# Performance work log

Measured on AMD Instinct MI355X. Metric: run time of the kernel, lower is better.

## Reference

```python
import jax, jax.numpy as jnp
import numpy as np

B, Q, K, H, V = 32, 64, 512, 64, 64
NEG = -1e6


def setup_inputs() -> dict:
    key = jax.random.key(0)
    ks = jax.random.split(key, 7)
    queries = jax.random.normal(ks[0], (B, Q, H), dtype=jnp.float32)
    keys = jax.random.normal(ks[1], (B, K, H), dtype=jnp.float32)
    values = jax.random.normal(ks[2], (B, K, V), dtype=jnp.float32)
    valid_lens = jax.random.randint(ks[3], (B,), 1, K + 1, dtype=jnp.int32)
    # Linear weights stored as (in_features, out_features); x @ W == torch Linear
    Wq = jax.random.normal(ks[4], (H, H), dtype=jnp.float32) / np.sqrt(H)
    Wk = jax.random.normal(ks[5], (H, H), dtype=jnp.float32) / np.sqrt(H)
    wv = jax.random.normal(ks[6], (H,), dtype=jnp.float32) / np.sqrt(H)
    return {"queries": queries, "keys": keys, "values": values,
            "valid_lens": valid_lens, "Wq": Wq, "Wk": Wk, "wv": wv}


def reference(queries, keys, values, valid_lens, Wq, Wk, wv):
    q = jnp.einsum('bqd,dh->bqh', queries, Wq)          # (B,Q,H)
    k = jnp.einsum('bkd,dh->bkh', keys, Wk)             # (B,K,H)
    # additive (Bahdanau) features: (B,Q,K,H) broadcast intermediate
    feats = jnp.tanh(q[:, :, None, :] + k[:, None, :, :])
    scores = jnp.einsum('bqkh,h->bqk', feats, wv)       # (B,Q,K)
    # masked softmax over key axis: positions >= valid_len get -1e6
    mask = jnp.arange(K)[None, :] < valid_lens[:, None]  # (B,K)
    scores = jnp.where(mask[:, None, :], scores, NEG)
    attn = jax.nn.softmax(scores, axis=-1)              # (B,Q,K)
    return jnp.einsum('bqk,bkv->bqv', attn, values)     # (B,Q,V)
```

## Files before the change

### kernel.cpp

```cpp
#include <hip/hip_runtime.h>
#include <hip/hip_bf16.h>

#define NEG (-1e6f)

static constexpr int B = 32, Q = 64, K = 512, H = 64, V = 64;
static constexpr float C2LE = 2.8853900817779268f;
static constexpr float L2E  = 1.4426950408889634f;

typedef __attribute__((ext_vector_type(8))) short bf16x8;
typedef __attribute__((ext_vector_type(4))) float f32x4;

__device__ __forceinline__ float fexp2(float x) { return __builtin_amdgcn_exp2f(x); }
__device__ __forceinline__ float frcp(float x)  { return __builtin_amdgcn_rcpf(x); }

__device__ __forceinline__ unsigned pk(float a, float b) {
  __hip_bfloat162 h = __float22bfloat162_rn(make_float2(a, b));
  return *reinterpret_cast<unsigned*>(&h);
}
union bfrag { unsigned u[4]; bf16x8 v; };

__global__ __launch_bounds__(256) void proj_kernel(
    const float* __restrict__ queries, const float* __restrict__ keys,
    const float* __restrict__ Wq, const float* __restrict__ Wk,
    const float* __restrict__ wv, const int* __restrict__ vlens,
    float* __restrict__ qAR2, unsigned* __restrict__ Ekp)
{
  __shared__ float Wl[64 * 65];
  const int xcd = blockIdx.x & 7, slot = blockIdx.x >> 3;
  const bool isQ = slot < 4;
  const int idx = slot - 4;
  const int b = isQ ? (xcd * 4 + slot) : (xcd * 4 + (idx & 3));
  const int kb64 = idx >> 2;
  const int vlen = vlens[b];
  if (!isQ && kb64 * 64 >= vlen) return;

  const int tid = threadIdx.x, lane = tid & 63;
  const int wave = __builtin_amdgcn_readfirstlane(tid >> 6);
  const float* Wsrc = isQ ? Wq : Wk;
  #pragma unroll
  for (int i = 0; i < 16; ++i) {
    const int j = tid + i * 256;
    Wl[(j >> 6) * 65 + (j & 63)] = Wsrc[j];
  }
  __syncthreads();

  const int r = lane & 15, g = lane >> 4;
  const int rloc0 = (isQ ? 0 : kb64 * 64) + wave * 16;
  if (!isQ && rloc0 >= vlen) return;
  const float* xbase = isQ ? (queries + ((size_t)b * Q + rloc0) * H)
                           : (keys    + ((size_t)b * K + rloc0) * H);

  bf16x8 afr[2];
  #pragma unroll
  for (int kb = 0; kb < 2; ++kb) {
    const float* px = xbase + (size_t)r * H + kb * 32 + g * 8;
    const float4 x0 = *(const float4*)px;
    const float4 x1 = *(const float4*)(px + 4);
    bfrag a;
    a.u[0] = pk(x0.x, x0.y); a.u[1] = pk(x0.z, x0.w);
    a.u[2] = pk(x1.x, x1.y); a.u[3] = pk(x1.z, x1.w);
    afr[kb] = a.v;
  }

  #pragma unroll
  for (int t = 0; t < 4; ++t) {
    const int hcol = t * 16 + r;
    f32x4 acc = {0.f, 0.f, 0.f, 0.f};
    #pragma unroll
    for (int kb = 0; kb < 2; ++kb) {
      const float* wp = &Wl[(kb * 32 + g * 8) * 65 + hcol];
      bfrag w;
      #pragma unroll
      for (int jj = 0; jj < 4; ++jj)
        w.u[jj] = pk(wp[(2*jj) * 65], wp[(2*jj + 1) * 65]);
      acc = isQ ? __builtin_amdgcn_mfma_f32_16x16x32_bf16(afr[kb], w.v, acc, 0, 0, 0)
                : __builtin_amdgcn_mfma_f32_16x16x32_bf16(w.v, afr[kb], acc, 0, 0, 0);
    }
    if (isQ) {
      const float wvv = wv[hcol];
      #pragma unroll
      for (int rr = 0; rr < 4; ++rr) {
        const int qq = rloc0 + g * 4 + rr;
        const float s = fminf(15.f, fmaxf(-15.f, acc[rr])) * C2LE;
        const float rq = fexp2(-s);
        const size_t off = (((size_t)(b * 16 + (qq >> 2)) * 32 + (hcol >> 1)) * 16)
                           + (qq & 3) * 4 + (hcol & 1) * 2;
        *(float2*)(qAR2 + off) = make_float2(-2.f * wvv * rq, rq);
      }
    } else {
      const int k = rloc0 + r;
      float E[4];
      #pragma unroll
      for (int rr = 0; rr < 4; ++rr)
        E[rr] = fexp2(fminf(15.f, fmaxf(-15.f, acc[rr])) * C2LE);
      const int hp = t * 8 + g * 2;
      Ekp[((size_t)b * 32 + hp    ) * 512 + k] = pk(E[0], E[1]);
      Ekp[((size_t)b * 32 + hp + 1) * 512 + k] = pk(E[2], E[3]);
    }
  }
}

__global__ __launch_bounds__(512) void attn_kernel(
    const float* __restrict__ qAR2, const unsigned* __restrict__ Ekp,
    const float* __restrict__ values, const int* __restrict__ vlens,
    float* __restrict__ out)
{
  __shared__ float p[4][K];
  __shared__ float part[8][4][V];
  __shared__ float red[4][2][2];

  const int xcd = blockIdx.x & 7, slot = blockIdx.x >> 3;
  const int b = xcd * 4 + (slot & 3), qg = slot >> 2;
  const int vlen = vlens[b];
  const int tid = threadIdx.x, lane = tid & 63;
  const int wave = __builtin_amdgcn_readfirstlane(tid >> 6);

  if (wave * 64 < vlen) {
    const unsigned* ekp = Ekp + (size_t)b * 32 * 512 + tid;
    const float* ar = qAR2 +
        (size_t)__builtin_amdgcn_readfirstlane((b * 16 + qg) * 512);
    unsigned ek[32];
    #pragma unroll
    for (int hp = 0; hp < 32; ++hp) ek[hp] = ekp[hp * 512];
    float a0 = 0.f, a1 = 0.f, a2 = 0.f, a3 = 0.f;
    #pragma unroll
    for (int hp = 0; hp < 32; ++hp) {
      const float E0 = __uint_as_float(ek[hp] << 16);
      const float E1 = __uint_as_float(ek[hp] & 0xffff0000u);
      const float* s = ar + hp * 16;
      a0 = fmaf(s[ 0], frcp(s[ 1] + E0), a0);
      a0 = fmaf(s[ 2], frcp(s[ 3] + E1), a0);
      a1 = fmaf(s[ 4], frcp(s[ 5] + E0), a1);
      a1 = fmaf(s[ 6], frcp(s[ 7] + E1), a1);
      a2 = fmaf(s[ 8], frcp(s[ 9] + E0), a2);
      a2 = fmaf(s[10], frcp(s[11] + E1), a2);
      a3 = fmaf(s[12], frcp(s[13] + E0), a3);
      a3 = fmaf(s[14], frcp(s[15] + E1), a3);
    }
    p[0][tid] = a0; p[1][tid] = a1; p[2][tid] = a2; p[3][tid] = a3;
  }
  __syncthreads();

  const int qi = wave & 3, half = wave >> 2;
  const int kb2 = half * 256 + lane * 4;
  {
    float s[4];
    *(float4*)s = *(const float4*)&p[qi][kb2];
    float m = NEG;
    #pragma unroll
    for (int j = 0; j < 4; ++j) {
      s[j] = (kb2 + j < vlen) ? s[j] : NEG;
      m = fmaxf(m, s[j]);
    }
    #pragma unroll
    for (int off = 32; off; off >>= 1) m = fmaxf(m, __shfl_xor(m, off, 64));
    if (lane == 0) red[qi][half][0] = m;
    __syncthreads();
    m = fmaxf(red[qi][0][0], red[qi][1][0]);
    float sum = 0.f;
    #pragma unroll
    for (int j = 0; j < 4; ++j) { s[j] = fexp2((s[j] - m) * L2E); sum += s[j]; }
    *(float4*)&p[qi][kb2] = *(float4*)s;
    #pragma unroll
    for (int off = 32; off; off >>= 1) sum += __shfl_xor(sum, off, 64);
    if (lane == 0) red[qi][half][1] = sum;
    __syncthreads();
  }

  {
    const int kb = wave * 64;
    if (kb < vlen) {
      const float* vb = values + ((size_t)b * K + kb) * V + lane;
      float a0 = 0.f, a1 = 0.f, a2 = 0.f, a3 = 0.f;
      #pragma unroll 4
      for (int k4 = 0; k4 < 64; k4 += 4) {
        const float4 p0 = *(const float4*)&p[0][kb + k4];
        const float4 p1 = *(const float4*)&p[1][kb + k4];
        const float4 p2 = *(const float4*)&p[2][kb + k4];
        const float4 p3 = *(const float4*)&p[3][kb + k4];
        const float v0 = vb[(size_t)(k4 + 0) * V];
        const float v1 = vb[(size_t)(k4 + 1) * V];
        const float v2 = vb[(size_t)(k4 + 2) * V];
        const float v3 = vb[(size_t)(k4 + 3) * V];
        a0 = fmaf(p0.x,v0, fmaf(p0.y,v1, fmaf(p0.z,v2, fmaf(p0.w,v3, a0))));
        a1 = fmaf(p1.x,v0, fmaf(p1.y,v1, fmaf(p1.z,v2, fmaf(p1.w,v3, a1))));
        a2 = fmaf(p2.x,v0, fmaf(p2.y,v1, fmaf(p2.z,v2, fmaf(p2.w,v3, a2))));
        a3 = fmaf(p3.x,v0, fmaf(p3.y,v1, fmaf(p3.z,v2, fmaf(p3.w,v3, a3))));
      }
      part[wave][0][lane] = a0; part[wave][1][lane] = a1;
      part[wave][2][lane] = a2; part[wave][3][lane] = a3;
    } else {
      part[wave][0][lane] = 0.f; part[wave][1][lane] = 0.f;
      part[wave][2][lane] = 0.f; part[wave][3][lane] = 0.f;
    }
  }
  __syncthreads();

  if (wave < 4) {
    const float inv = frcp(red[wave][0][1] + red[wave][1][1]);
    float o = 0.f;
    #pragma unroll
    for (int w = 0; w < 8; ++w) o += part[w][wave][lane];
    out[((size_t)b * Q + qg * 4 + wave) * V + lane] = o * inv;
  }
}

extern "C" void kernel_launch(void* const* d_in, const int* in_sizes, int n_in,
                              void* d_out, int out_size, void* d_ws, size_t ws_size,
                              hipStream_t stream) {
  const float* queries = (const float*)d_in[0];
  const float* keys    = (const float*)d_in[1];
  const float* values  = (const float*)d_in[2];
  const int*   vlens   = (const int*)d_in[3];
  const float* Wq      = (const float*)d_in[4];
  const float* Wk      = (const float*)d_in[5];
  const float* wv      = (const float*)d_in[6];
  float* out = (float*)d_out;

  float*    qAR2 = (float*)d_ws;
  unsigned* Ekp  = (unsigned*)(qAR2 + (size_t)B*16*512);

  proj_kernel<<<288, 256, 0, stream>>>(queries, keys, Wq, Wk, wv, vlens, qAR2, Ekp);
  attn_kernel<<<512, 512, 0, stream>>>(qAR2, Ekp, values, vlens, out);
}
```

Baseline: 23.67 us.

## Use per-XCD atomic work queue with one query per task in attention

The attention kernel becomes a persistent loop. Blocks pull (batch, query) tasks from a per-XCD atomic counter instead of each block statically handling four queries. The aim is to balance work across batches with uneven valid lengths, and the qAR2 layout changes to a per-query stride to match. In exchange, each task reloads its 32 Ekp words per thread and pays three block barriers plus an atomic per query. A memset launch is also added to reset the queue counters.

```diff
diff --git a/kernel.cpp b/kernel.cpp
--- a/kernel.cpp
+++ b/kernel.cpp
@@ -83,8 +83,8 @@
         const int qq = rloc0 + g * 4 + rr;
         const float s = fminf(15.f, fmaxf(-15.f, acc[rr])) * C2LE;
         const float rq = fexp2(-s);
-        const size_t off = (((size_t)(b * 16 + (qq >> 2)) * 32 + (hcol >> 1)) * 16)
-                           + (qq & 3) * 4 + (hcol & 1) * 2;
+        const size_t off = ((size_t)(b * 64 + qq) * 32 + (hcol >> 1)) * 4
+                           + (hcol & 1) * 2;
         *(float2*)(qAR2 + off) = make_float2(-2.f * wvv * rq, rq);
       }
     } else {
@@ -103,105 +103,84 @@
 __global__ __launch_bounds__(512) void attn_kernel(
     const float* __restrict__ qAR2, const unsigned* __restrict__ Ekp,
     const float* __restrict__ values, const int* __restrict__ vlens,
-    float* __restrict__ out)
+    int* __restrict__ queue, float* __restrict__ out)
 {
-  __shared__ float p[4][K];
-  __shared__ float part[8][4][V];
-  __shared__ float red[4][2][2];
-
-  const int xcd = blockIdx.x & 7, slot = blockIdx.x >> 3;
-  const int b = xcd * 4 + (slot & 3), qg = slot >> 2;
-  const int vlen = vlens[b];
+  __shared__ float p[K];
+  __shared__ float part[8][V];
+  __shared__ float red[8][2];
+  __shared__ int task_sh;
+
   const int tid = threadIdx.x, lane = tid & 63;
   const int wave = __builtin_amdgcn_readfirstlane(tid >> 6);
-
-  if (wave * 64 < vlen) {
-    const unsigned* ekp = Ekp + (size_t)b * 32 * 512 + tid;
-    const float* ar = qAR2 +
-        (size_t)__builtin_amdgcn_readfirstlane((b * 16 + qg) * 512);
-    unsigned ek[32];
-    #pragma unroll
-    for (int hp = 0; hp < 32; ++hp) ek[hp] = ekp[hp * 512];
-    float a0 = 0.f, a1 = 0.f, a2 = 0.f, a3 = 0.f;
-    #pragma unroll
-    for (int hp = 0; hp < 32; ++hp) {
-      const float E0 = __uint_as_float(ek[hp] << 16);
-      const float E1 = __uint_as_float(ek[hp] & 0xffff0000u);
-      const float* s = ar + hp * 16;
-      a0 = fmaf(s[ 0], frcp(s[ 1] + E0), a0);
-      a0 = fmaf(s[ 2], frcp(s[ 3] + E1), a0);
-      a1 = fmaf(s[ 4], frcp(s[ 5] + E0), a1);
-      a1 = fmaf(s[ 6], frcp(s[ 7] + E1), a1);
-      a2 = fmaf(s[ 8], frcp(s[ 9] + E0), a2);
-      a2 = fmaf(s[10], frcp(s[11] + E1), a2);
-      a3 = fmaf(s[12], frcp(s[13] + E0), a3);
-      a3 = fmaf(s[14], frcp(s[15] + E1), a3);
-    }
-    p[0][tid] = a0; p[1][tid] = a1; p[2][tid] = a2; p[3][tid] = a3;
-  }
-  __syncthreads();
-
-  const int qi = wave & 3, half = wave >> 2;
-  const int kb2 = half * 256 + lane * 4;
-  {
-    float s[4];
-    *(float4*)s = *(const float4*)&p[qi][kb2];
-    float m = NEG;
-    #pragma unroll
-    for (int j = 0; j < 4; ++j) {
-      s[j] = (kb2 + j < vlen) ? s[j] : NEG;
-      m = fmaxf(m, s[j]);
-    }
+  const int xcd = blockIdx.x & 7;
+
+  for (;;) {
+    if (tid == 0) task_sh = atomicAdd(&queue[xcd], 1);
+    __syncthreads();
+    const int t = task_sh;
+    if (t >= 256) break;
+    const int b = xcd * 4 + (t & 3), q = t >> 2;
+    const int vlen = vlens[b];
+
+    float a0 = 0.f;
+    if (wave * 64 < vlen) {
+      const unsigned* ekp = Ekp + (size_t)b * 32 * 512 + tid;
+      const float* ar = qAR2 +
+          (size_t)__builtin_amdgcn_readfirstlane((b * 64 + q) * 128);
+      unsigned ek[32];
+      #pragma unroll
+      for (int hp = 0; hp < 32; ++hp) ek[hp] = ekp[hp * 512];
+      #pragma unroll
+      for (int hp = 0; hp < 32; ++hp) {
+        const float E0 = __uint_as_float(ek[hp] << 16);
+        const float E1 = __uint_as_float(ek[hp] & 0xffff0000u);
+        const float* s = ar + hp * 4;
+        a0 = fmaf(s[0], frcp(s[1] + E0), a0);
+        a0 = fmaf(s[2], frcp(s[3] + E1), a0);
+      }
+    }
+
+    const float am = (tid < vlen) ? a0 : NEG;
+    float m = am;
     #pragma unroll
     for (int off = 32; off; off >>= 1) m = fmaxf(m, __shfl_xor(m, off, 64));
-    if (lane == 0) red[qi][half][0] = m;
-    __syncthreads();
-    m = fmaxf(red[qi][0][0], red[qi][1][0]);
-    float sum = 0.f;
-    #pragma unroll
-    for (int j = 0; j < 4; ++j) { s[j] = fexp2((s[j] - m) * L2E); sum += s[j]; }
-    *(float4*)&p[qi][kb2] = *(float4*)s;
+    if (lane == 0) red[wave][0] = m;
+    __syncthreads();
+    float gm = red[0][0];
+    #pragma unroll
+    for (int w = 1; w < 8; ++w) gm = fmaxf(gm, red[w][0]);
+    const float pexp = fexp2((am - gm) * L2E);
+    p[tid] = pexp;
+    float sum = pexp;
     #pragma unroll
     for (int off = 32; off; off >>= 1) sum += __shfl_xor(sum, off, 64);
-    if (lane == 0) red[qi][half][1] = sum;
-    __syncthreads();
-  }
-
-  {
+    if (lane == 0) red[wave][1] = sum;
+    __syncthreads();
+
+    float c = 0.f;
     const int kb = wave * 64;
     if (kb < vlen) {
       const float* vb = values + ((size_t)b * K + kb) * V + lane;
-      float a0 = 0.f, a1 = 0.f, a2 = 0.f, a3 = 0.f;
       #pragma unroll 4
       for (int k4 = 0; k4 < 64; k4 += 4) {
-        const float4 p0 = *(const float4*)&p[0][kb + k4];
-        const float4 p1 = *(const float4*)&p[1][kb + k4];
-        const float4 p2 = *(const float4*)&p[2][kb + k4];
-        const float4 p3 = *(const float4*)&p[3][kb + k4];
-        const float v0 = vb[(size_t)(k4 + 0) * V];
-        const float v1 = vb[(size_t)(k4 + 1) * V];
-        const float v2 = vb[(size_t)(k4 + 2) * V];
-        const float v3 = vb[(size_t)(k4 + 3) * V];
-        a0 = fmaf(p0.x,v0, fmaf(p0.y,v1, fmaf(p0.z,v2, fmaf(p0.w,v3, a0))));
-        a1 = fmaf(p1.x,v0, fmaf(p1.y,v1, fmaf(p1.z,v2, fmaf(p1.w,v3, a1))));
-        a2 = fmaf(p2.x,v0, fmaf(p2.y,v1, fmaf(p2.z,v2, fmaf(p2.w,v3, a2))));
-        a3 = fmaf(p3.x,v0, fmaf(p3.y,v1, fmaf(p3.z,v2, fmaf(p3.w,v3, a3))));
+        const float4 p4 = *(const float4*)&p[kb + k4];
+        c = fmaf(p4.x, vb[(size_t)(k4 + 0) * V], c);
+        c = fmaf(p4.y, vb[(size_t)(k4 + 1) * V], c);
+        c = fmaf(p4.z, vb[(size_t)(k4 + 2) * V], c);
+        c = fmaf(p4.w, vb[(size_t)(k4 + 3) * V], c);
       }
-      part[wave][0][lane] = a0; part[wave][1][lane] = a1;
-      part[wave][2][lane] = a2; part[wave][3][lane] = a3;
-    } else {
-      part[wave][0][lane] = 0.f; part[wave][1][lane] = 0.f;
-      part[wave][2][lane] = 0.f; part[wave][3][lane] = 0.f;
-    }
-  }
-  __syncthreads();
-
-  if (wave < 4) {
-    const float inv = frcp(red[wave][0][1] + red[wave][1][1]);
-    float o = 0.f;
-    #pragma unroll
-    for (int w = 0; w < 8; ++w) o += part[w][wave][lane];
-    out[((size_t)b * Q + qg * 4 + wave) * V + lane] = o * inv;
+    }
+    part[wave][lane] = c;
+    __syncthreads();
+
+    if (wave == 0) {
+      const float gsum = red[0][1] + red[1][1] + red[2][1] + red[3][1] +
+                         red[4][1] + red[5][1] + red[6][1] + red[7][1];
+      float o = 0.f;
+      #pragma unroll
+      for (int w = 0; w < 8; ++w) o += part[w][lane];
+      out[((size_t)b * Q + q) * V + lane] = o * frcp(gsum);
+    }
   }
 }
 
@@ -218,8 +197,10 @@
   float* out = (float*)d_out;
 
   float*    qAR2 = (float*)d_ws;
-  unsigned* Ekp  = (unsigned*)(qAR2 + (size_t)B*16*512);
-
+  unsigned* Ekp  = (unsigned*)(qAR2 + (size_t)B*64*128);
+  int*      queue = (int*)(Ekp + (size_t)B*32*512);
+
+  hipMemsetAsync(queue, 0, 8 * sizeof(int), stream);
   proj_kernel<<<288, 256, 0, stream>>>(queries, keys, Wq, Wk, wv, vlens, qAR2, Ekp);
-  attn_kernel<<<512, 512, 0, stream>>>(qAR2, Ekp, values, vlens, out);
-}
+  attn_kernel<<<1024, 512, 0, stream>>>(qAR2, Ekp, values, vlens, queue, out);
+}
```

Measured after the change: 52.23 us. 2.21x slower.

## Stage Ek tile in LDS, rebalance PV over valid keys, swizzle batch mapping

Applied to the files above, without the earlier changes.

The attention kernel first copies the per-batch packed Ek table (32x512) into shared memory with 16-byte cooperative loads, skipping the half beyond the valid length, instead of each thread issuing 32 strided global loads. The shared buffer is then reused for the probability and partial-sum arrays. The P·V stage now splits only the valid key range, rounded to a multiple of 32, evenly across the 8 waves instead of fixed 64-key slices. A slot-dependent rotation changes which batch each block handles. The cost is a 64KB LDS footprint that limits occupancy, plus extra barriers.

```diff
diff --git a/kernel.cpp b/kernel.cpp
--- a/kernel.cpp
+++ b/kernel.cpp
@@ -105,28 +105,38 @@
     const float* __restrict__ values, const int* __restrict__ vlens,
     float* __restrict__ out)
 {
-  __shared__ float p[4][K];
-  __shared__ float part[8][4][V];
+  __shared__ unsigned ekl[32 * 512];
   __shared__ float red[4][2][2];
 
   const int xcd = blockIdx.x & 7, slot = blockIdx.x >> 3;
-  const int b = xcd * 4 + (slot & 3), qg = slot >> 2;
+  const int b  = xcd * 4 + ((slot + (slot >> 5)) & 3);
+  const int qg = slot >> 2;
   const int vlen = vlens[b];
   const int tid = threadIdx.x, lane = tid & 63;
   const int wave = __builtin_amdgcn_readfirstlane(tid >> 6);
 
+  {
+    const unsigned* src = Ekp + (size_t)b * 32 * 512;
+    #pragma unroll
+    for (int i = 0; i < 8; ++i) {
+      const int c = i * 8 + wave;
+      if ((c & 1) * 256 < vlen) {
+        const uint4 v = *(const uint4*)(src + c * 256 + lane * 4);
+        *(uint4*)&ekl[c * 256 + lane * 4] = v;
+      }
+    }
+  }
+  __syncthreads();
+
+  float a0 = 0.f, a1 = 0.f, a2 = 0.f, a3 = 0.f;
   if (wave * 64 < vlen) {
-    const unsigned* ekp = Ekp + (size_t)b * 32 * 512 + tid;
     const float* ar = qAR2 +
         (size_t)__builtin_amdgcn_readfirstlane((b * 16 + qg) * 512);
-    unsigned ek[32];
-    #pragma unroll
-    for (int hp = 0; hp < 32; ++hp) ek[hp] = ekp[hp * 512];
-    float a0 = 0.f, a1 = 0.f, a2 = 0.f, a3 = 0.f;
     #pragma unroll
     for (int hp = 0; hp < 32; ++hp) {
-      const float E0 = __uint_as_float(ek[hp] << 16);
-      const float E1 = __uint_as_float(ek[hp] & 0xffff0000u);
+      const unsigned u = ekl[hp * 512 + tid];
+      const float E0 = __uint_as_float(u << 16);
+      const float E1 = __uint_as_float(u & 0xffff0000u);
       const float* s = ar + hp * 16;
       a0 = fmaf(s[ 0], frcp(s[ 1] + E0), a0);
       a0 = fmaf(s[ 2], frcp(s[ 3] + E1), a0);
@@ -137,7 +147,13 @@
       a3 = fmaf(s[12], frcp(s[13] + E0), a3);
       a3 = fmaf(s[14], frcp(s[15] + E1), a3);
     }
-    p[0][tid] = a0; p[1][tid] = a1; p[2][tid] = a2; p[3][tid] = a3;
+  }
+  __syncthreads();
+  float* p    = (float*)ekl;
+  float* part = (float*)ekl + 2048;
+  if (wave * 64 < vlen) {
+    p[0 * 512 + tid] = a0; p[1 * 512 + tid] = a1;
+    p[2 * 512 + tid] = a2; p[3 * 512 + tid] = a3;
   }
   __syncthreads();
 
@@ -145,7 +161,7 @@
   const int kb2 = half * 256 + lane * 4;
   {
     float s[4];
-    *(float4*)s = *(const float4*)&p[qi][kb2];
+    *(float4*)s = *(const float4*)&p[qi * 512 + kb2];
     float m = NEG;
     #pragma unroll
     for (int j = 0; j < 4; ++j) {
@@ -160,7 +176,7 @@
     float sum = 0.f;
     #pragma unroll
     for (int j = 0; j < 4; ++j) { s[j] = fexp2((s[j] - m) * L2E); sum += s[j]; }
-    *(float4*)&p[qi][kb2] = *(float4*)s;
+    *(float4*)&p[qi * 512 + kb2] = *(float4*)s;
     #pragma unroll
     for (int off = 32; off; off >>= 1) sum += __shfl_xor(sum, off, 64);
     if (lane == 0) red[qi][half][1] = sum;
@@ -168,31 +184,27 @@
   }
 
   {
-    const int kb = wave * 64;
-    if (kb < vlen) {
-      const float* vb = values + ((size_t)b * K + kb) * V + lane;
-      float a0 = 0.f, a1 = 0.f, a2 = 0.f, a3 = 0.f;
-      #pragma unroll 4
-      for (int k4 = 0; k4 < 64; k4 += 4) {
-        const float4 p0 = *(const float4*)&p[0][kb + k4];
-        const float4 p1 = *(const float4*)&p[1][kb + k4];
-        const float4 p2 = *(const float4*)&p[2][kb + k4];
-        const float4 p3 = *(const float4*)&p[3][kb + k4];
-        const float v0 = vb[(size_t)(k4 + 0) * V];
-        const float v1 = vb[(size_t)(k4 + 1) * V];
-        const float v2 = vb[(size_t)(k4 + 2) * V];
-        const float v3 = vb[(size_t)(k4 + 3) * V];
-        a0 = fmaf(p0.x,v0, fmaf(p0.y,v1, fmaf(p0.z,v2, fmaf(p0.w,v3, a0))));
-        a1 = fmaf(p1.x,v0, fmaf(p1.y,v1, fmaf(p1.z,v2, fmaf(p1.w,v3, a1))));
-        a2 = fmaf(p2.x,v0, fmaf(p2.y,v1, fmaf(p2.z,v2, fmaf(p2.w,v3, a2))));
-        a3 = fmaf(p3.x,v0, fmaf(p3.y,v1, fmaf(p3.z,v2, fmaf(p3.w,v3, a3))));
-      }
-      part[wave][0][lane] = a0; part[wave][1][lane] = a1;
-      part[wave][2][lane] = a2; part[wave][3][lane] = a3;
-    } else {
-      part[wave][0][lane] = 0.f; part[wave][1][lane] = 0.f;
-      part[wave][2][lane] = 0.f; part[wave][3][lane] = 0.f;
-    }
+    const int chunk = ((vlen + 31) >> 5) << 2;
+    const int kb = wave * chunk;
+    const float* vb = values + ((size_t)b * K + kb) * V + lane;
+    float c0 = 0.f, c1 = 0.f, c2 = 0.f, c3 = 0.f;
+    #pragma unroll 4
+    for (int k4 = 0; k4 < chunk; k4 += 4) {
+      const float4 p0 = *(const float4*)&p[0 * 512 + kb + k4];
+      const float4 p1 = *(const float4*)&p[1 * 512 + kb + k4];
+      const float4 p2 = *(const float4*)&p[2 * 512 + kb + k4];
+      const float4 p3 = *(const float4*)&p[3 * 512 + kb + k4];
+      const float v0 = vb[(size_t)(k4 + 0) * V];
+      const float v1 = vb[(size_t)(k4 + 1) * V];
+      const float v2 = vb[(size_t)(k4 + 2) * V];
+      const float v3 = vb[(size_t)(k4 + 3) * V];
+      c0 = fmaf(p0.x,v0, fmaf(p0.y,v1, fmaf(p0.z,v2, fmaf(p0.w,v3, c0))));
+      c1 = fmaf(p1.x,v0, fmaf(p1.y,v1, fmaf(p1.z,v2, fmaf(p1.w,v3, c1))));
+      c2 = fmaf(p2.x,v0, fmaf(p2.y,v1, fmaf(p2.z,v2, fmaf(p2.w,v3, c2))));
+      c3 = fmaf(p3.x,v0, fmaf(p3.y,v1, fmaf(p3.z,v2, fmaf(p3.w,v3, c3))));
+    }
+    part[(wave*4+0)*64+lane] = c0; part[(wave*4+1)*64+lane] = c1;
+    part[(wave*4+2)*64+lane] = c2; part[(wave*4+3)*64+lane] = c3;
   }
   __syncthreads();
 
@@ -200,7 +212,7 @@
     const float inv = frcp(red[wave][0][1] + red[wave][1][1]);
     float o = 0.f;
     #pragma unroll
-    for (int w = 0; w < 8; ++w) o += part[w][wave][lane];
+    for (int w = 0; w < 8; ++w) o += part[(w*4+wave)*64 + lane];
     out[((size_t)b * Q + qg * 4 + wave) * V + lane] = o * inv;
   }
 }
```

Measured after the change: 23.61 us. About the same (-0.3%).
